# Optimization experiments

Measured on AMD Instinct MI355X. Metric: run time of the kernel, lower is better.

Reference implementation:

```python
import jax, jax.numpy as jnp
import numpy as np

C = 256  # input_channels == output_channels (residual add requires it)
EPS = 1e-5


def conv1d(x, w, b):
    # x: [B, Cin, L], w: [Cout, Cin, K], 'same' padding for K=3,p=1
    y = jax.lax.conv_general_dilated(x, w, window_strides=(1,), padding=[(1, 1)],
                                     dimension_numbers=('NCH', 'OIH', 'NCH'))
    return y + b[None, :, None]


def batchnorm(x, gamma, beta):
    # training-mode BN over (batch, length) per channel, biased variance
    m = jnp.mean(x, axis=(0, 2), keepdims=True)
    v = jnp.var(x, axis=(0, 2), keepdims=True)
    return (x - m) * jax.lax.rsqrt(v + EPS) * gamma[None, :, None] + beta[None, :, None]


def cross_attn(q_in, kv_in, res, qw, qb, kw, kb, vw, vb, ow, ob, g, be):
    q = conv1d(q_in, qw, qb)   # [B, C, L]
    k = conv1d(kv_in, kw, kb)  # [B, C, L]
    v = conv1d(kv_in, vw, vb)  # [B, C, L]
    scores = jnp.einsum('bcl,bcm->blm', q, k) / jnp.sqrt(jnp.float32(C))
    probs = jax.nn.softmax(scores, axis=-1)          # [B, L, L]
    ctx = jnp.einsum('blm,bcm->bcl', probs, v)       # [B, C, L]
    return batchnorm(conv1d(ctx, ow, ob), g, be) + res


def setup_inputs() -> dict:
    key = jax.random.key(0)
    ks = jax.random.split(key, 24)
    B, L = 16, 1024
    d = {
        'image': jax.random.normal(ks[0], (B, C, L), jnp.float32),
        'clinical': jax.random.normal(ks[1], (B, 1, L), jnp.float32),
    }
    def w(k, shape):
        return jax.random.normal(k, shape, jnp.float32) * 0.05
    # branch a: cli_to_img (query from image, key/value from clinical)
    d['a_qw'] = w(ks[2], (C, C, 3)); d['a_qb'] = w(ks[3], (C,))
    d['a_kw'] = w(ks[4], (C, 1, 3)); d['a_kb'] = w(ks[5], (C,))
    d['a_vw'] = w(ks[6], (C, 1, 3)); d['a_vb'] = w(ks[7], (C,))
    d['a_ow'] = w(ks[8], (C, C, 3)); d['a_ob'] = w(ks[9], (C,))
    d['a_g'] = jnp.ones((C,), jnp.float32); d['a_beta'] = jnp.zeros((C,), jnp.float32)
    # branch b: img_to_cli (query from clinical, key/value from image)
    d['b_qw'] = w(ks[10], (C, 1, 3)); d['b_qb'] = w(ks[11], (C,))
    d['b_kw'] = w(ks[12], (C, C, 3)); d['b_kb'] = w(ks[13], (C,))
    d['b_vw'] = w(ks[14], (C, C, 3)); d['b_vb'] = w(ks[15], (C,))
    d['b_ow'] = w(ks[16], (C, C, 3)); d['b_ob'] = w(ks[17], (C,))
    d['b_g'] = jnp.ones((C,), jnp.float32); d['b_beta'] = jnp.zeros((C,), jnp.float32)
    return d


def reference(image, clinical,
              a_qw, a_qb, a_kw, a_kb, a_vw, a_vb, a_ow, a_ob, a_g, a_beta,
              b_qw, b_qb, b_kw, b_kb, b_vw, b_vb, b_ow, b_ob, b_g, b_beta):
    cli_to_img = cross_attn(image, clinical, image,
                            a_qw, a_qb, a_kw, a_kb, a_vw, a_vb, a_ow, a_ob, a_g, a_beta)
    img_to_cli = cross_attn(clinical, image, image,
                            b_qw, b_qb, b_kw, b_kb, b_vw, b_vb, b_ow, b_ob, b_g, b_beta)
    return jnp.concatenate([cli_to_img, img_to_cli], axis=1)  # [B, 2C, L]
```

## Files before the change

kernel.cpp:

```cpp
#include <hip/hip_runtime.h>


typedef short bf16x8 __attribute__((ext_vector_type(8)));
typedef float f32x4 __attribute__((ext_vector_type(4)));

__device__ __forceinline__ unsigned short f2bf(float f) {
    union { float f; unsigned u; } v; v.f = f;
    unsigned r = v.u + 0x7fffu + ((v.u >> 16) & 1u);
    return (unsigned short)(r >> 16);
}
__device__ __forceinline__ float bf2f(unsigned short h) {
    union { unsigned u; float f; } v; v.u = ((unsigned)h) << 16;
    return v.f;
}

__device__ __forceinline__ void glds16(const void* g, void* l) {
    __builtin_amdgcn_global_load_lds(
        (const __attribute__((address_space(1))) unsigned int*)g,
        (__attribute__((address_space(3))) unsigned int*)l, 16, 0, 0);
}

#define TM 128
#define TN 128
#define BK 32

struct GOp {
    const unsigned short* A; const unsigned short* B; void* C;
    long sA, sB, sC;
    int lda, ldb, ldc, nxt, nyt, nz, K;
    const float* bias_row; const float* bias_col;
    const float* row_scale;
    float* stats; int stat_base;
};

__global__ __launch_bounds__(256)
void gemm_nt(GOp op0, GOp op1, int n0, float alpha)
{
    __shared__ __attribute__((aligned(16))) char sh[34816];
    unsigned short* shs = (unsigned short*)sh;
    int id = blockIdx.x;
    const bool brn = (id >= n0);
    const GOp op = brn ? op1 : op0;
    if (brn) id -= n0;
    const int bz = id % op.nz;
    const int rem = id / op.nz;
    const int by = rem / op.nxt;
    const int bx = rem - by * op.nxt;

    const unsigned short* Ab = op.A + op.sA * bz;
    const unsigned short* Bb = op.B + op.sB * bz;
    const int lda = op.lda, ldb = op.ldb;
    const int i0 = by * TM;
    const int j0 = bx * TN;
    const int t = threadIdx.x;
    const int lane = t & 63;
    const int wave = t >> 6;
    const int wm = wave & 1, wn = wave >> 1;

    const int srow = wave * 16 + (lane >> 2);
    const int sc8 = (lane & 3) * 8;
    const unsigned short* gA0 = Ab + (long)(i0 + srow) * lda + sc8;
    const unsigned short* gA1 = gA0 + (long)64 * lda;
    const unsigned short* gB0 = Bb + (long)(j0 + srow) * ldb + sc8;
    const unsigned short* gB1 = gB0 + (long)64 * ldb;
    const int d0 = wave * 512;
    const int d1 = 2048 + wave * 512;

    f32x4 acc[4][4];
#pragma unroll
    for (int a_ = 0; a_ < 4; ++a_)
#pragma unroll
        for (int b_ = 0; b_ < 4; ++b_)
            acc[a_][b_] = (f32x4){0.f, 0.f, 0.f, 0.f};

    const int frow = lane & 15;
    const int fk = (lane >> 4) * 8;

    glds16(gA0, shs + d0);
    glds16(gA1, shs + d1);
    glds16(gB0, shs + 8192 + d0);
    glds16(gB1, shs + 8192 + d1);

    int cur = 0;
    for (int k0 = 0; k0 < op.K; k0 += BK) {
        __syncthreads();
        const int kn = k0 + BK;
        if (kn < op.K) {
            const int nb = cur ^ 1;
            glds16(gA0 + kn, shs + nb * 4096 + d0);
            glds16(gA1 + kn, shs + nb * 4096 + d1);
            glds16(gB0 + kn, shs + 8192 + nb * 4096 + d0);
            glds16(gB1 + kn, shs + 8192 + nb * 4096 + d1);
        }
        const unsigned short* la = shs + cur * 4096;
        const unsigned short* lb = shs + 8192 + cur * 4096;
        bf16x8 af[4], bfr[4];
#pragma unroll
        for (int mt = 0; mt < 4; ++mt)
            af[mt] = *(const bf16x8*)(&la[(wm * 64 + mt * 16 + frow) * BK + fk]);
#pragma unroll
        for (int nt = 0; nt < 4; ++nt)
            bfr[nt] = *(const bf16x8*)(&lb[(wn * 64 + nt * 16 + frow) * BK + fk]);
#pragma unroll
        for (int mt = 0; mt < 4; ++mt)
#pragma unroll
            for (int nt = 0; nt < 4; ++nt)
                acc[mt][nt] = __builtin_amdgcn_mfma_f32_16x16x32_bf16(af[mt], bfr[nt], acc[mt][nt], 0, 0, 0);
        cur ^= 1;
    }

    const int lr = (lane >> 4) * 4;
    const int lc = lane & 15;
    __syncthreads();

    unsigned short* tile = shs;
#pragma unroll
    for (int mt = 0; mt < 4; ++mt) {
#pragma unroll
        for (int nt = 0; nt < 4; ++nt) {
            const int col = wn * 64 + nt * 16 + lc;
            const float bc = op.bias_col ? op.bias_col[j0 + col] : 0.f;
#pragma unroll
            for (int r = 0; r < 4; ++r) {
                const int row = wm * 64 + mt * 16 + lr + r;
                const float brv = op.bias_row ? op.bias_row[i0 + row] : 0.f;
                const float rsv = op.row_scale
                    ? op.row_scale[(long)bz * (op.nyt * TM) + i0 + row] : 1.f;
                tile[row * 136 + col] = f2bf((acc[mt][nt][r] * alpha + brv + bc) * rsv);
            }
        }
    }
    __syncthreads();
    unsigned short* Cb = (unsigned short*)op.C + op.sC * bz;
#pragma unroll
    for (int p = 0; p < 8; ++p) {
        const int cid = p * 256 + t;
        const int row = cid >> 4;
        const int c8 = (cid & 15) * 8;
        const uint4 v = *(const uint4*)(tile + row * 136 + c8);
        *(uint4*)(Cb + (long)(i0 + row) * op.ldc + j0 + c8) = v;
    }
    if (op.stats) {
        const int row = t >> 1, half = t & 1;
        float s = 0.f, s2 = 0.f;
#pragma unroll
        for (int c = 0; c < 64; c += 8) {
            const bf16x8 v = *(const bf16x8*)(tile + row * 136 + half * 64 + c);
#pragma unroll
            for (int e = 0; e < 8; ++e) {
                const float f = bf2f((unsigned short)v[e]);
                s += f; s2 += f * f;
            }
        }
        s += __shfl_xor(s, 1);
        s2 += __shfl_xor(s2, 1);
        if (half == 0) {
            const int ch = op.stat_base + i0 + row;
            atomicAdd(&op.stats[ch], s);
            atomicAdd(&op.stats[512 + ch], s2);
        }
    }
}

__global__ __launch_bounds__(256)
void mats(const unsigned short* __restrict__ QK,
          const float* __restrict__ a_kw, const float* __restrict__ a_kb,
          const float* __restrict__ b_qw, const float* __restrict__ b_qb,
          float* __restrict__ M4A, float* __restrict__ M4Y)
{
    const int z = blockIdx.x >> 2;
    const int l = ((blockIdx.x & 3) << 8) + threadIdx.x;
    const unsigned short* row = QK + ((long)z * 1024 + l) * 512;
    float a0 = 0.f, a1 = 0.f, a2 = 0.f, d = 0.f;
    float y0 = 0.f, y1 = 0.f, y2 = 0.f, cb = 0.f;
    for (int c8 = 0; c8 < 32; ++c8) {
        const bf16x8 q = *(const bf16x8*)(row + c8 * 8);
        const bf16x8 k = *(const bf16x8*)(row + 256 + c8 * 8);
#pragma unroll
        for (int e = 0; e < 8; ++e) {
            const int c = c8 * 8 + e;
            const float qv = bf2f((unsigned short)q[e]);
            const float kv = bf2f((unsigned short)k[e]);
            a0 += qv * a_kw[c * 3];     a1 += qv * a_kw[c * 3 + 1];
            a2 += qv * a_kw[c * 3 + 2]; d  += qv * a_kb[c];
            y0 += kv * b_qw[c * 3];     y1 += kv * b_qw[c * 3 + 1];
            y2 += kv * b_qw[c * 3 + 2]; cb += kv * b_qb[c];
        }
    }
    const long o = ((long)z * 1024 + l) * 4;
    *(float4*)(M4A + o) = make_float4(a0, a1, a2, d);
    *(float4*)(M4Y + o) = make_float4(y0, y1, y2, cb);
}

__global__ __launch_bounds__(256)
void attn_mid(const float* __restrict__ cli,
              const float* __restrict__ M4A, const float* __restrict__ M4Y,
              const float* __restrict__ a_vw, const float* __restrict__ a_vb,
              unsigned short* __restrict__ P, float* __restrict__ invl,
              unsigned short* __restrict__ ctxT)
{
    __shared__ __attribute__((aligned(16))) char smem[38912];
    const int bid = blockIdx.x;
    const int t = threadIdx.x;
    if (bid < 64) {
        const int z = bid >> 2;
        const int l0 = (bid & 3) << 8;
        float* xs = (float*)smem;
        for (int i = t; i < 1026; i += 256) {
            const int l = i - 1;
            xs[i] = (l >= 0 && l < 1024) ? cli[(long)z * 1024 + l] : 0.f;
        }
        __syncthreads();
        const float4 A = *(const float4*)(M4A + ((long)z * 1024 + l0 + t) * 4);
        float t0a = 0.f, t1a = 0.f, t2a = 0.f, lsa = 0.f;
        float t0b = 0.f, t1b = 0.f, t2b = 0.f, lsb = 0.f;
#pragma unroll 8
        for (int m = 0; m < 1024; m += 2) {
            const float x0 = xs[m],     x1 = xs[m + 1], x2 = xs[m + 2];
            const float u0 = xs[m + 1], u1 = xs[m + 2], u2 = xs[m + 3];
            const float e0 = __expf((A.x * x0 + A.y * x1 + A.z * x2 + A.w) * 0.0625f);
            const float e1 = __expf((A.x * u0 + A.y * u1 + A.z * u2 + A.w) * 0.0625f);
            t0a += e0 * x0; t1a += e0 * x1; t2a += e0 * x2; lsa += e0;
            t0b += e1 * u0; t1b += e1 * u1; t2b += e1 * u2; lsb += e1;
        }
        const float inv = 1.f / (lsa + lsb);
        const float th0 = (t0a + t0b) * inv, th1 = (t1a + t1b) * inv,
                    th2 = (t2a + t2b) * inv;
        __syncthreads();
        float* tt = (float*)smem;
        *(float4*)(tt + t * 4) = make_float4(th0, th1, th2, 0.f);
        __syncthreads();
        const float wv0 = a_vw[t * 3], wv1 = a_vw[t * 3 + 1], wv2 = a_vw[t * 3 + 2];
        const float bv = a_vb[t];
        unsigned short* Ob = ctxT + ((long)z * 1026 + 1 + l0) * 256;
        for (int l = 0; l < 256; ++l) {
            const float4 th = *(const float4*)(tt + l * 4);
            Ob[(long)l * 256 + t] = f2bf(wv0 * th.x + wv1 * th.y + wv2 * th.z + bv);
        }
    } else {
        const int b2 = bid - 64;
        const int z = b2 >> 4;
        const int l0 = (b2 & 15) << 6;
        float* xs = (float*)smem;
        float* ys = (float*)(smem + 512);
        unsigned short* Pt = (unsigned short*)(smem + 4608);
        if (t < 66) {
            const int l = l0 + t - 1;
            xs[t] = (l >= 0 && l < 1024) ? cli[(long)z * 1024 + l] : 0.f;
        }
        const int li = t >> 2, mg = t & 3;
        unsigned short* Pg = P + (long)z * 1024 * 1024;
        float lsum = 0.f;
        float x0 = 0.f, x1 = 0.f, x2 = 0.f;
        for (int mc = 0; mc < 4; ++mc) {
            __syncthreads();
            *(float4*)(ys + t * 4) =
                *(const float4*)(M4Y + ((long)z * 1024 + mc * 256 + t) * 4);
            __syncthreads();
            if (mc == 0) { x0 = xs[li]; x1 = xs[li + 1]; x2 = xs[li + 2]; }
#pragma unroll
            for (int i8 = 0; i8 < 8; ++i8) {
                bf16x8 out;
#pragma unroll
                for (int e = 0; e < 8; ++e) {
                    const int m = mg * 64 + i8 * 8 + e;
                    const float4 y = *(const float4*)(ys + m * 4);
                    const float p =
                        __expf((x0 * y.x + x1 * y.y + x2 * y.z + y.w) * 0.0625f);
                    lsum += p;
                    out[e] = (short)f2bf(p);
                }
                *(bf16x8*)(Pt + li * 260 + mg * 64 + i8 * 8) = out;
            }
            __syncthreads();
#pragma unroll
            for (int p8 = 0; p8 < 8; ++p8) {
                const int cid = p8 * 256 + t;
                const int row = cid >> 5, c8 = (cid & 31) * 8;
                *(uint4*)(Pg + (long)(l0 + row) * 1024 + mc * 256 + c8) =
                    *(const uint4*)(Pt + row * 260 + c8);
            }
        }
        lsum += __shfl_xor(lsum, 1);
        lsum += __shfl_xor(lsum, 2);
        if (mg == 0)
            invl[(long)z * 1024 + l0 + li] = 1.f / lsum;
    }
}

__global__ __launch_bounds__(256)
void prep(const float* __restrict__ image,
          const float* __restrict__ a_qw, const float* __restrict__ a_qb,
          const float* __restrict__ b_kw, const float* __restrict__ b_kb,
          const float* __restrict__ b_vw,
          const float* __restrict__ a_ow, const float* __restrict__ b_ow,
          unsigned short* __restrict__ imgT, unsigned short* __restrict__ ctxT,
          unsigned short* __restrict__ W, float* __restrict__ qkb,
          float* __restrict__ sums)
{
    __shared__ char smem[64 * 65 * 4];
    const int b = blockIdx.x;
    const int t = threadIdx.x;
    if (b < 1024) {
        float* tile = (float*)smem;
        const int bt = b >> 6, rem = b & 63;
        const int l0 = (rem & 15) * 64, c0 = (rem >> 4) * 64;
        const float* xb = image + ((long)bt * 256 + c0) * 1024 + l0;
        for (int idx = t; idx < 4096; idx += 256) {
            const int cc = idx >> 6, ll = idx & 63;
            tile[cc * 65 + ll] = xb[(long)cc * 1024 + ll];
        }
        __syncthreads();
        unsigned short* op = imgT + ((long)bt * 1026 + l0 + 1) * 256 + c0;
        for (int idx = t; idx < 4096; idx += 256) {
            const int ll = idx >> 6, cc = idx & 63;
            op[(long)ll * 256 + cc] = f2bf(tile[cc * 65 + ll]);
        }
    } else if (b < 4864) {
        const int i = (b - 1024) * 256 + t;
        const int row = i / 768;
        const int kk = i - row * 768;
        const int j = kk >> 8, ci = kk & 255;
        const float* src = (row < 256) ? a_qw : (row < 512) ? b_kw
                         : (row < 768) ? b_vw : (row < 1024) ? a_ow : b_ow;
        const int r = row & 255;
        W[i] = f2bf(src[r * 768 + ci * 3 + j]);
    } else {
        const int i = (b - 4864) * 256 + t;
        if (i < 512) {
            qkb[i] = (i < 256) ? a_qb[i] : b_kb[i - 256];
        } else if (i < 512 + 8192) {
            const int p = i - 512;
            const int bi = p >> 9, rr = (p >> 8) & 1, c = p & 255;
            imgT[((long)bi * 1026 + (rr ? 1025 : 0)) * 256 + c] = 0;
        } else if (i < 512 + 8192 + 16384) {
            const int p = i - 512 - 8192;
            const int bz = p >> 9, rr = (p >> 8) & 1, c = p & 255;
            ctxT[((long)bz * 1026 + (rr ? 1025 : 0)) * 256 + c] = 0;
        } else if (i < 512 + 8192 + 16384 + 1024) {
            sums[i - 512 - 8192 - 16384] = 0.f;
        }
    }
}

__global__ __launch_bounds__(256)
void bn_finalize(const float* __restrict__ sums,
                 const float* __restrict__ ag, const float* __restrict__ abeta,
                 const float* __restrict__ bg, const float* __restrict__ bbeta,
                 float* __restrict__ ss)
{
    const int ch = blockIdx.x * 256 + threadIdx.x;
    const int branch = ch >> 8, c = ch & 255;
    const float mean = sums[ch] * (1.f / 16384.f);
    const float var = sums[512 + ch] * (1.f / 16384.f) - mean * mean;
    const float inv = rsqrtf(var + 1e-5f);
    const float g = branch ? bg[c] : ag[c];
    const float be = branch ? bbeta[c] : abeta[c];
    const float sc = g * inv;
    ss[ch] = sc;
    ss[512 + ch] = be - mean * sc;
}

__global__ __launch_bounds__(256)
void bn_apply(const unsigned short* __restrict__ Y, const float* __restrict__ img,
              const float* __restrict__ ss, float* __restrict__ out)
{
    const long i4 = (long)blockIdx.x * 256 + threadIdx.x;
    const long e = i4 * 4;
    const int l = (int)(e & 1023);
    const int ch = (int)((e >> 10) & 511);
    const int b = (int)(e >> 19);
    const int branch = ch >> 8, c = ch & 255;
    const float sc = ss[ch], sh = ss[512 + ch];
    const long yoff = (((long)(branch * 16 + b)) * 256 + c) * 1024 + l;
    const long ioff = ((long)b * 256 + c) * 1024 + l;
    const ushort4 yv = *(const ushort4*)(Y + yoff);
    const float4 iv = *(const float4*)(img + ioff);
    float4 o;
    o.x = bf2f(yv.x) * sc + sh + iv.x;
    o.y = bf2f(yv.y) * sc + sh + iv.y;
    o.z = bf2f(yv.z) * sc + sh + iv.z;
    o.w = bf2f(yv.w) * sc + sh + iv.w;
    *(float4*)(out + e) = o;
}

extern "C" void kernel_launch(void* const* d_in, const int* in_sizes, int n_in,
                              void* d_out, int out_size, void* d_ws, size_t ws_size,
                              hipStream_t stream)
{
    const float* image    = (const float*)d_in[0];
    const float* clinical = (const float*)d_in[1];
    const float* a_qw = (const float*)d_in[2];  const float* a_qb = (const float*)d_in[3];
    const float* a_kw = (const float*)d_in[4];  const float* a_kb = (const float*)d_in[5];
    const float* a_vw = (const float*)d_in[6];  const float* a_vb = (const float*)d_in[7];
    const float* a_ow = (const float*)d_in[8];  const float* a_ob = (const float*)d_in[9];
    const float* a_g  = (const float*)d_in[10]; const float* a_be = (const float*)d_in[11];
    const float* b_qw = (const float*)d_in[12]; const float* b_qb = (const float*)d_in[13];
    const float* b_kw = (const float*)d_in[14]; const float* b_kb = (const float*)d_in[15];
    const float* b_vw = (const float*)d_in[16]; const float* b_vb = (const float*)d_in[17];
    const float* b_ow = (const float*)d_in[18]; const float* b_ob = (const float*)d_in[19];
    const float* b_g  = (const float*)d_in[20]; const float* b_be = (const float*)d_in[21];
    float* out = (float*)d_out;

    char* ws = (char*)d_ws;
    const long MB = 1048576L;
    unsigned short* imgT = (unsigned short*)(ws);
    unsigned short* ctxT = (unsigned short*)(ws + 9 * MB);
    unsigned short* vb   = (unsigned short*)(ws + 54 * MB);
    unsigned short* QK   = (unsigned short*)(ws + 62 * MB);
    unsigned short* P    = (unsigned short*)(ws + 80 * MB);
    float*          M4A  = (float*)(ws + 114 * MB);
    float*          M4Y  = (float*)(ws + 115 * MB);
    float*          invl = (float*)(ws + 116 * MB);
    unsigned short* Y    = (unsigned short*)(ws + 142 * MB);
    unsigned short* W    = (unsigned short*)(ws + 174 * MB);
    float*          qkb  = (float*)(ws + 176 * MB);
    float*          ss   = qkb + 512;
    float*          sums = qkb + 1536;
    unsigned short* Wqk = W;
    unsigned short* Wvb = W + 512L * 768;
    unsigned short* Woa = W + 768L * 768;
    unsigned short* Wob = W + 1024L * 768;

    const dim3 blk(256);
    const long sIT = 1026L * 256, sQK = 1024L * 512, sV = 256L * 1024;
    const long sP = 1024L * 1024;

    prep<<<4966, blk, 0, stream>>>(image, a_qw, a_qb, b_kw, b_kb, b_vw,
                                   a_ow, b_ow, imgT, ctxT, W, qkb, sums);
    {
        GOp opQ = {imgT, Wqk, QK, sIT, 0, sQK, 256, 768, 512, 4, 8, 16, 768,
                   nullptr, qkb, nullptr, nullptr, 0};
        GOp opV = {Wvb, imgT, vb, 0, sIT, sV, 768, 256, 1024, 8, 2, 16, 768,
                   b_vb, nullptr, nullptr, nullptr, 0};
        gemm_nt<<<768, blk, 0, stream>>>(opQ, opV, 512, 1.f);
    }
    mats<<<64, blk, 0, stream>>>(QK, a_kw, a_kb, b_qw, b_qb, M4A, M4Y);
    attn_mid<<<320, blk, 0, stream>>>(clinical, M4A, M4Y, a_vw, a_vb,
                                      P, invl, ctxT);
    {
        GOp opA = {Woa, ctxT, Y, 0, sIT, sV, 768, 256, 1024, 8, 2, 16, 768,
                   a_ob, nullptr, nullptr, sums, 0};
        GOp opPV = {P, vb, ctxT + 16 * sIT + 256, sP, sV, sIT, 1024, 1024, 256,
                    2, 8, 16, 1024, nullptr, nullptr, invl, nullptr, 0};
        gemm_nt<<<512, blk, 0, stream>>>(opA, opPV, 256, 1.f);
    }
    {
        GOp opB = {Wob, ctxT + 16 * sIT, Y + 16 * sV, 0, sIT, sV, 768, 256, 1024,
                   8, 2, 16, 768, b_ob, nullptr, nullptr, sums, 256};
        gemm_nt<<<256, blk, 0, stream>>>(opB, opB, 256, 1.f);
    }
    bn_finalize<<<2, blk, 0, stream>>>(sums, a_g, a_be, b_g, b_be, ss);
    bn_apply<<<8192, blk, 0, stream>>>(Y, image, ss, out);
}
```

Before: 276.0 us.

## Split attn_mid work across more blocks and write P rows directly

The branch-a part now gives each row to four lanes that split the key dimension and combine with shuffles, so 256 blocks of 64 rows replace 64 blocks of 256 rows. The branch-b part now uses 16 threads per row and 16-row blocks. It reads M4Y straight from global memory and stores bf16 P rows directly, with no LDS staging or block barriers. The grid grows from 320 to 1280 blocks to fill the GPU better. The cost is redundant global/L2 reads of M4Y and less coalesced P stores, since each thread writes 16-byte chunks at a 32-element stride.

```diff
diff --git a/kernel.cpp b/kernel.cpp
--- a/kernel.cpp
+++ b/kernel.cpp
@@ -199,92 +199,73 @@
               unsigned short* __restrict__ P, float* __restrict__ invl,
               unsigned short* __restrict__ ctxT)
 {
-    __shared__ __attribute__((aligned(16))) char smem[38912];
+    __shared__ __attribute__((aligned(16))) float smem[1032 + 256];
     const int bid = blockIdx.x;
     const int t = threadIdx.x;
-    if (bid < 64) {
-        const int z = bid >> 2;
-        const int l0 = (bid & 3) << 8;
-        float* xs = (float*)smem;
+    if (bid < 256) {
+        const int z = bid & 15;
+        const int l0 = (bid >> 4) << 6;
+        float* xs = smem;
+        float* tt = smem + 1032;
         for (int i = t; i < 1026; i += 256) {
             const int l = i - 1;
             xs[i] = (l >= 0 && l < 1024) ? cli[(long)z * 1024 + l] : 0.f;
         }
         __syncthreads();
-        const float4 A = *(const float4*)(M4A + ((long)z * 1024 + l0 + t) * 4);
-        float t0a = 0.f, t1a = 0.f, t2a = 0.f, lsa = 0.f;
-        float t0b = 0.f, t1b = 0.f, t2b = 0.f, lsb = 0.f;
-#pragma unroll 8
-        for (int m = 0; m < 1024; m += 2) {
-            const float x0 = xs[m],     x1 = xs[m + 1], x2 = xs[m + 2];
-            const float u0 = xs[m + 1], u1 = xs[m + 2], u2 = xs[m + 3];
-            const float e0 = __expf((A.x * x0 + A.y * x1 + A.z * x2 + A.w) * 0.0625f);
-            const float e1 = __expf((A.x * u0 + A.y * u1 + A.z * u2 + A.w) * 0.0625f);
-            t0a += e0 * x0; t1a += e0 * x1; t2a += e0 * x2; lsa += e0;
-            t0b += e1 * u0; t1b += e1 * u1; t2b += e1 * u2; lsb += e1;
-        }
-        const float inv = 1.f / (lsa + lsb);
-        const float th0 = (t0a + t0b) * inv, th1 = (t1a + t1b) * inv,
-                    th2 = (t2a + t2b) * inv;
-        __syncthreads();
-        float* tt = (float*)smem;
-        *(float4*)(tt + t * 4) = make_float4(th0, th1, th2, 0.f);
+        const int r = t >> 2, q = t & 3;
+        const float4 A = *(const float4*)(M4A + ((long)z * 1024 + l0 + r) * 4);
+        float t0 = 0.f, t1 = 0.f, t2 = 0.f, ls = 0.f;
+        const int m0 = q * 256;
+#pragma unroll 4
+        for (int m = m0; m < m0 + 256; ++m) {
+            const float x0 = xs[m], x1 = xs[m + 1], x2 = xs[m + 2];
+            const float e = __expf((A.x * x0 + A.y * x1 + A.z * x2 + A.w) * 0.0625f);
+            t0 += e * x0; t1 += e * x1; t2 += e * x2; ls += e;
+        }
+        t0 += __shfl_xor(t0, 1); t0 += __shfl_xor(t0, 2);
+        t1 += __shfl_xor(t1, 1); t1 += __shfl_xor(t1, 2);
+        t2 += __shfl_xor(t2, 1); t2 += __shfl_xor(t2, 2);
+        ls += __shfl_xor(ls, 1); ls += __shfl_xor(ls, 2);
+        if (q == 0) *(float4*)(tt + r * 4) = make_float4(t0, t1, t2, ls);
         __syncthreads();
         const float wv0 = a_vw[t * 3], wv1 = a_vw[t * 3 + 1], wv2 = a_vw[t * 3 + 2];
         const float bv = a_vb[t];
         unsigned short* Ob = ctxT + ((long)z * 1026 + 1 + l0) * 256;
-        for (int l = 0; l < 256; ++l) {
-            const float4 th = *(const float4*)(tt + l * 4);
-            Ob[(long)l * 256 + t] = f2bf(wv0 * th.x + wv1 * th.y + wv2 * th.z + bv);
+        for (int rr = 0; rr < 64; ++rr) {
+            const float4 th = *(const float4*)(tt + rr * 4);
+            const float inv = 1.f / th.w;
+            Ob[(long)rr * 256 + t] = f2bf((wv0 * th.x + wv1 * th.y + wv2 * th.z) * inv + bv);
         }
     } else {
-        const int b2 = bid - 64;
-        const int z = b2 >> 4;
-        const int l0 = (b2 & 15) << 6;
-        float* xs = (float*)smem;
-        float* ys = (float*)(smem + 512);
-        unsigned short* Pt = (unsigned short*)(smem + 4608);
-        if (t < 66) {
-            const int l = l0 + t - 1;
-            xs[t] = (l >= 0 && l < 1024) ? cli[(long)z * 1024 + l] : 0.f;
-        }
-        const int li = t >> 2, mg = t & 3;
-        unsigned short* Pg = P + (long)z * 1024 * 1024;
+        const int b2 = bid - 256;
+        const int z = b2 & 15;
+        const int l0 = (b2 >> 4) << 4;
+        const int li = t >> 4, mg = t & 15;
+        const int l = l0 + li;
+        const float x0 = (l >= 1) ? cli[(long)z * 1024 + l - 1] : 0.f;
+        const float x1 = cli[(long)z * 1024 + l];
+        const float x2 = (l < 1023) ? cli[(long)z * 1024 + l + 1] : 0.f;
+        const float4* Yz = (const float4*)(M4Y + (long)z * 4096);
+        unsigned short* Pr = P + ((long)z * 1024 + l) * 1024;
         float lsum = 0.f;
-        float x0 = 0.f, x1 = 0.f, x2 = 0.f;
-        for (int mc = 0; mc < 4; ++mc) {
-            __syncthreads();
-            *(float4*)(ys + t * 4) =
-                *(const float4*)(M4Y + ((long)z * 1024 + mc * 256 + t) * 4);
-            __syncthreads();
-            if (mc == 0) { x0 = xs[li]; x1 = xs[li + 1]; x2 = xs[li + 2]; }
-#pragma unroll
-            for (int i8 = 0; i8 < 8; ++i8) {
+#pragma unroll
+        for (int jc = 0; jc < 4; ++jc)
+#pragma unroll
+            for (int i8 = 0; i8 < 2; ++i8) {
+                const int mb = jc * 256 + mg * 16 + i8 * 8;
                 bf16x8 out;
 #pragma unroll
                 for (int e = 0; e < 8; ++e) {
-                    const int m = mg * 64 + i8 * 8 + e;
-                    const float4 y = *(const float4*)(ys + m * 4);
-                    const float p =
-                        __expf((x0 * y.x + x1 * y.y + x2 * y.z + y.w) * 0.0625f);
+                    const float4 y = Yz[mb + e];
+                    const float p = __expf((x0 * y.x + x1 * y.y + x2 * y.z + y.w) * 0.0625f);
                     lsum += p;
                     out[e] = (short)f2bf(p);
                 }
-                *(bf16x8*)(Pt + li * 260 + mg * 64 + i8 * 8) = out;
+                *(bf16x8*)(Pr + mb) = out;
             }
-            __syncthreads();
-#pragma unroll
-            for (int p8 = 0; p8 < 8; ++p8) {
-                const int cid = p8 * 256 + t;
-                const int row = cid >> 5, c8 = (cid & 31) * 8;
-                *(uint4*)(Pg + (long)(l0 + row) * 1024 + mc * 256 + c8) =
-                    *(const uint4*)(Pt + row * 260 + c8);
-            }
-        }
-        lsum += __shfl_xor(lsum, 1);
-        lsum += __shfl_xor(lsum, 2);
-        if (mg == 0)
-            invl[(long)z * 1024 + l0 + li] = 1.f / lsum;
+        lsum += __shfl_xor(lsum, 1); lsum += __shfl_xor(lsum, 2);
+        lsum += __shfl_xor(lsum, 4); lsum += __shfl_xor(lsum, 8);
+        if (mg == 0) invl[(long)z * 1024 + l] = 1.f / lsum;
     }
 }
 
@@ -436,8 +417,8 @@
         gemm_nt<<<768, blk, 0, stream>>>(opQ, opV, 512, 1.f);
     }
     mats<<<64, blk, 0, stream>>>(QK, a_kw, a_kb, b_qw, b_qb, M4A, M4Y);
-    attn_mid<<<320, blk, 0, stream>>>(clinical, M4A, M4Y, a_vw, a_vb,
-                                      P, invl, ctxT);
+    attn_mid<<<1280, blk, 0, stream>>>(clinical, M4A, M4Y, a_vw, a_vb,
+                                       P, invl, ctxT);
     {
         GOp opA = {Woa, ctxT, Y, 0, sIT, sV, 768, 256, 1024, 8, 2, 16, 768,
                    a_ob, nullptr, nullptr, sums, 0};
```

After: 266.5 us. 1.04x faster.
